# Kernel optimization log

Measured on AMD Instinct MI355X. Metric: run time of the kernel, lower is better.

Reference implementation:

```python
import jax, jax.numpy as jnp
import numpy as np

N = 100000
E = 1600000
IN_FEATS = 128
HIDDEN = 128
CLASSES = 64


def setup_inputs() -> dict:
    key = jax.random.key(0)
    ks = jax.random.split(key, 8)
    features = jax.random.normal(ks[0], (N, IN_FEATS), dtype=jnp.float32)
    edge_index = jax.random.randint(ks[1], (2, E), 0, N, dtype=jnp.int64 if jax.config.jax_enable_x64 else jnp.int32)
    # Glorot-init weights like PyG's GCNConv.lin, zero bias
    def glorot(k, fan_in, fan_out):
        lim = (6.0 / (fan_in + fan_out)) ** 0.5
        return jax.random.uniform(k, (fan_in, fan_out), dtype=jnp.float32, minval=-lim, maxval=lim)
    return {
        "features": features,
        "edge_index": edge_index,
        "W1": glorot(ks[2], IN_FEATS, HIDDEN), "b1": jnp.zeros((HIDDEN,), jnp.float32),
        "W2": glorot(ks[3], HIDDEN, HIDDEN), "b2": jnp.zeros((HIDDEN,), jnp.float32),
        "W3": glorot(ks[4], HIDDEN, CLASSES), "b3": jnp.zeros((CLASSES,), jnp.float32),
    }


def _gcn_conv(x, W, b, row, col, deg_norm_row, deg_norm_col):
    # x: [N, d_in] -> [N, d_out]. PyG GCNConv: linear first, then normalized aggregation, then bias.
    xw = x @ W                                   # [N, d_out]
    norm = deg_norm_row * deg_norm_col          # [E]
    msg = norm[:, None] * xw[row]               # gather from source nodes
    out = jax.ops.segment_sum(msg, col, num_segments=N)  # scatter-add to dst
    return out + b


def reference(features, edge_index, W1, b1, W2, b2, W3, b3):
    row, col = edge_index[0], edge_index[1]  # source -> target
    # gcn_norm with add_self_loops=False, unit edge weights: deg over dst nodes
    deg = jax.ops.segment_sum(jnp.ones((E,), features.dtype), col, num_segments=N)
    dinv = jnp.where(deg > 0, jax.lax.rsqrt(jnp.maximum(deg, 1.0)), 0.0)
    dn_row, dn_col = dinv[row], dinv[col]
    h = jax.nn.relu(_gcn_conv(features, W1, b1, row, col, dn_row, dn_col))
    h = jax.nn.relu(_gcn_conv(h, W2, b2, row, col, dn_row, dn_col))
    h = jax.nn.relu(_gcn_conv(h, W3, b3, row, col, dn_row, dn_col))
    return h
```

## Files before the change

### kernel.cpp

```cpp
#include <hip/hip_runtime.h>

#define ALIGNUP(x) (((x) + 255) & ~(size_t)255)
#define ABLK 256
#define BSHIFT 9

typedef _Float16 f16x8 __attribute__((ext_vector_type(8)));
typedef float f32x4 __attribute__((ext_vector_type(4)));


__global__ void bucket_hist_kernel(const int* __restrict__ col, unsigned* __restrict__ gHist,
                                   int nE, int chunk) {
    __shared__ unsigned hist[256];
    const int tid = threadIdx.x, blk = blockIdx.x;
    hist[tid] = 0;
    __syncthreads();
    const int e0 = blk * chunk, e1 = min(nE, e0 + chunk);
    for (int e = e0 + tid; e < e1; e += 256)
        atomicAdd(&hist[((unsigned)col[e]) >> BSHIFT], 1u);
    __syncthreads();
    gHist[tid * ABLK + blk] = hist[tid];
}

__global__ void bucket_scan_kernel(unsigned* __restrict__ g) {
    __shared__ unsigned ps[1024];
    const int tid = threadIdx.x;
    const int base = tid * 64;
    unsigned sum = 0;
    for (int k = 0; k < 64; ++k) sum += g[base + k];
    ps[tid] = sum;
    __syncthreads();
    for (int o = 1; o < 1024; o <<= 1) {
        unsigned t = tid >= o ? ps[tid - o] : 0u;
        __syncthreads();
        ps[tid] += t;
        __syncthreads();
    }
    unsigned run = ps[tid] - sum;
    for (int k = 0; k < 64; ++k) {
        unsigned v = g[base + k];
        g[base + k] = run;
        run += v;
    }
}

__global__ void bucket_scatter_kernel(const int* __restrict__ row, const int* __restrict__ col,
                                      const unsigned* __restrict__ gScan,
                                      unsigned* __restrict__ pairs, int nE, int chunk) {
    __shared__ unsigned basec[256];
    const int tid = threadIdx.x, blk = blockIdx.x;
    basec[tid] = gScan[tid * ABLK + blk];
    __syncthreads();
    const int e0 = blk * chunk, e1 = min(nE, e0 + chunk);
    for (int e = e0 + tid; e < e1; e += 256) {
        unsigned d = (unsigned)col[e];
        unsigned pos = atomicAdd(&basec[d >> BSHIFT], 1u);
        pairs[pos] = (((unsigned)row[e]) << BSHIFT) | (d & 511u);
    }
}

__global__ void bucket_sort_kernel(const unsigned* __restrict__ pairs,
                                   const unsigned* __restrict__ gScan,
                                   int* __restrict__ srcs, int* __restrict__ off,
                                   float* __restrict__ dinv, int nN, int nE) {
    __shared__ unsigned cnt[512], sc[512];
    const int tid = threadIdx.x, b = blockIdx.x;
    const unsigned s = gScan[b * ABLK];
    const unsigned t = (b + 1 < 256) ? gScan[(b + 1) * ABLK] : (unsigned)nE;
    cnt[tid] = 0;
    __syncthreads();
    for (unsigned i = s + tid; i < t; i += 512)
        atomicAdd(&cnt[pairs[i] & 511u], 1u);
    __syncthreads();
    const unsigned v = cnt[tid];
    sc[tid] = v;
    __syncthreads();
    for (int o = 1; o < 512; o <<= 1) {
        unsigned q = tid >= o ? sc[tid - o] : 0u;
        __syncthreads();
        sc[tid] += q;
        __syncthreads();
    }
    const unsigned excl = sc[tid] - v;
    const int node = b * 512 + tid;
    if (node < nN) {
        dinv[node] = v > 0 ? rsqrtf((float)v) : 0.f;
        off[node] = (int)(s + excl);
    }
    if (b == 0 && tid == 0) off[nN] = nE;
    sc[tid] = excl;
    __syncthreads();
    for (unsigned i = s + tid; i < t; i += 512) {
        unsigned p = pairs[i];
        unsigned pos = s + atomicAdd(&sc[p & 511u], 1u);
        srcs[pos] = (int)(p >> BSHIFT);
    }
}


template <int DOUT>
__global__ void wf_prep_kernel(const float* __restrict__ W, f16x8* __restrict__ Wf) {
    const int c = blockIdx.x * blockDim.x + threadIdx.x;
    if (c >= DOUT * 16) return;
    const int l = c & 63;
    const int fk = (c >> 6) & 3;
    const int j = c >> 8;
    const int n = j * 16 + (l & 15);
    const int kbase = fk * 32 + ((l >> 4) * 8);
    f16x8 v;
#pragma unroll
    for (int e = 0; e < 8; ++e)
        v[e] = (_Float16)W[(size_t)(kbase + e) * DOUT + n];
    Wf[c] = v;
}


template <int DOUT, bool AF32>
__launch_bounds__(256)
__global__ void gemm_mfma(const void* __restrict__ Xv, const f16x8* __restrict__ Wf,
                          const float* __restrict__ dinv, _Float16* __restrict__ Y, int nrows) {
    constexpr int NTILE = DOUT / 16;
    const int lane = threadIdx.x & 63;
    const int wvid = threadIdx.x >> 6;
    const int m = lane & 15;
    const int kb = lane >> 4;
    const int r0 = blockIdx.x * 64 + wvid * 16;
    if (r0 >= nrows) return;
    const int arow = min(r0 + m, nrows - 1);

    f16x8 a[4];
    if constexpr (AF32) {
        const float* Xp = (const float*)Xv + (size_t)arow * 128 + kb * 8;
#pragma unroll
        for (int k = 0; k < 4; ++k) {
            const float4 x0 = *(const float4*)(Xp + k * 32);
            const float4 x1 = *(const float4*)(Xp + k * 32 + 4);
            f16x8 t;
            t[0] = (_Float16)x0.x; t[1] = (_Float16)x0.y;
            t[2] = (_Float16)x0.z; t[3] = (_Float16)x0.w;
            t[4] = (_Float16)x1.x; t[5] = (_Float16)x1.y;
            t[6] = (_Float16)x1.z; t[7] = (_Float16)x1.w;
            a[k] = t;
        }
    } else {
        const _Float16* Xp = (const _Float16*)Xv + (size_t)arow * 128 + kb * 8;
#pragma unroll
        for (int k = 0; k < 4; ++k) a[k] = *(const f16x8*)(Xp + k * 32);
    }

    f32x4 acc[NTILE];
#pragma unroll
    for (int j = 0; j < NTILE; ++j) acc[j] = (f32x4){0.f, 0.f, 0.f, 0.f};
#pragma unroll
    for (int k = 0; k < 4; ++k)
#pragma unroll
        for (int j = 0; j < NTILE; ++j)
            acc[j] = __builtin_amdgcn_mfma_f32_16x16x32_f16(
                         a[k], Wf[(j * 4 + k) * 64 + lane], acc[j], 0, 0, 0);

#pragma unroll
    for (int i = 0; i < 4; ++i) {
        const int r = r0 + kb * 4 + i;
        if (r < nrows) {
            const float dv = dinv[r];
#pragma unroll
            for (int j = 0; j < NTILE; ++j)
                Y[(size_t)r * DOUT + j * 16 + m] = (_Float16)(acc[j][i] * dv);
        }
    }
}


template <int LD, typename OT>
__launch_bounds__(256)
__global__ void gather_grp(const _Float16* __restrict__ XW, const int* __restrict__ off,
                           const int* __restrict__ srcs, const float* __restrict__ dinv,
                           const float* __restrict__ bias, OT* __restrict__ out, int nN) {
    constexpr int G = 8, GPW = 8;
    const int half = blockIdx.y;
    XW   += half * 64;
    bias += half * 64;
    out  += half * 64;
    const int lane = threadIdx.x & 63;
    const int gl   = lane % G;
    const int grp  = lane / G;
    const int wid  = (blockIdx.x * blockDim.x + threadIdx.x) >> 6;
    const int nw   = (gridDim.x * blockDim.x) >> 6;

    for (int v0 = wid * GPW; v0 < nN; v0 += nw * GPW) {
        const int v   = v0 + grp;
        const bool act = v < nN;
        const int s0 = act ? off[v] : 0;
        const int s1 = act ? off[v + 1] : 0;
        float acc[8];
#pragma unroll
        for (int k = 0; k < 8; ++k) acc[k] = 0.f;

        int base = s0;
        while (base + G <= s1) {
            const int myidx = srcs[base + gl];
#pragma unroll
            for (int j = 0; j < G; ++j) {
                const int src = __shfl(myidx, grp * G + j);
                union { uint4 u; _Float16 h[8]; } cv;
                cv.u = *(const uint4*)(XW + (size_t)src * LD + gl * 8);
#pragma unroll
                for (int k = 0; k < 8; ++k) acc[k] += (float)cv.h[k];
            }
            base += G;
        }
        if (base < s1) {
            const int myidx = srcs[min(base + gl, s1 - 1)];
            const int rem = s1 - base;
            for (int j = 0; j < rem; ++j) {
                const int src = __shfl(myidx, grp * G + j);
                union { uint4 u; _Float16 h[8]; } cv;
                cv.u = *(const uint4*)(XW + (size_t)src * LD + gl * 8);
#pragma unroll
                for (int k = 0; k < 8; ++k) acc[k] += (float)cv.h[k];
            }
        }

        if (act) {
            const float dv = dinv[v];
            const float4 b0 = ((const float4*)bias)[gl * 2];
            const float4 b1 = ((const float4*)bias)[gl * 2 + 1];
            float o[8];
            o[0] = fmaxf(dv * acc[0] + b0.x, 0.f);
            o[1] = fmaxf(dv * acc[1] + b0.y, 0.f);
            o[2] = fmaxf(dv * acc[2] + b0.z, 0.f);
            o[3] = fmaxf(dv * acc[3] + b0.w, 0.f);
            o[4] = fmaxf(dv * acc[4] + b1.x, 0.f);
            o[5] = fmaxf(dv * acc[5] + b1.y, 0.f);
            o[6] = fmaxf(dv * acc[6] + b1.z, 0.f);
            o[7] = fmaxf(dv * acc[7] + b1.w, 0.f);
            if constexpr (sizeof(OT) == 2) {
                union { uint4 u; _Float16 h[8]; } ov;
#pragma unroll
                for (int k = 0; k < 8; ++k) ov.h[k] = (_Float16)o[k];
                *(uint4*)((_Float16*)out + (size_t)v * LD + gl * 8) = ov.u;
            } else {
                float* op = (float*)out + (size_t)v * LD + gl * 8;
                *(float4*)op       = make_float4(o[0], o[1], o[2], o[3]);
                *(float4*)(op + 4) = make_float4(o[4], o[5], o[6], o[7]);
            }
        }
    }
}

extern "C" void kernel_launch(void* const* d_in, const int* in_sizes, int n_in,
                              void* d_out, int out_size, void* d_ws, size_t ws_size,
                              hipStream_t stream) {
    const float* feats = (const float*)d_in[0];
    const int*   ei    = (const int*)d_in[1];
    const float* W1    = (const float*)d_in[2];
    const float* b1    = (const float*)d_in[3];
    const float* W2    = (const float*)d_in[4];
    const float* b2    = (const float*)d_in[5];
    const float* W3    = (const float*)d_in[6];
    const float* b3    = (const float*)d_in[7];

    const int N = in_sizes[0] / 128;
    const int E = in_sizes[1] / 2;
    const int* row = ei;
    const int* col = ei + E;

    char* p = (char*)d_ws;
    unsigned* gHist = (unsigned*)p; p += ALIGNUP((size_t)256 * ABLK * 4);
    float*     dinv = (float*)p;    p += ALIGNUP((size_t)N * 4);
    int*       off  = (int*)p;      p += ALIGNUP((size_t)(N + 1) * 4);
    int*       srcs = (int*)p;      p += ALIGNUP((size_t)E * 4);
    f16x8*     wf1  = (f16x8*)p;    p += ALIGNUP((size_t)128 * 16 * 16);
    f16x8*     wf2  = (f16x8*)p;    p += ALIGNUP((size_t)128 * 16 * 16);
    f16x8*     wf3  = (f16x8*)p;    p += ALIGNUP((size_t)64 * 16 * 16);
    _Float16*  bufW = (_Float16*)p; p += ALIGNUP((size_t)N * 128 * 2);
    _Float16*  bufX = (_Float16*)p;
    unsigned* pairs = (unsigned*)bufX;

    wf_prep_kernel<128><<<8, 256, 0, stream>>>(W1, wf1);
    wf_prep_kernel<128><<<8, 256, 0, stream>>>(W2, wf2);
    wf_prep_kernel<64><<<4, 256, 0, stream>>>(W3, wf3);

    const int chunk = (E + ABLK - 1) / ABLK;
    const int NB    = (N + 511) >> BSHIFT;
    bucket_hist_kernel<<<ABLK, 256, 0, stream>>>(col, gHist, E, chunk);
    bucket_scan_kernel<<<1, 1024, 0, stream>>>(gHist);
    bucket_scatter_kernel<<<ABLK, 256, 0, stream>>>(row, col, gHist, pairs, E, chunk);
    bucket_sort_kernel<<<NB, 512, 0, stream>>>(pairs, gHist, srcs, off, dinv, N, E);

    const int NCH = (N + 63) / 64;
    const int GBg = (N + 31) / 32;

    gemm_mfma<128, true><<<NCH, 256, 0, stream>>>(feats, wf1, dinv, bufW, N);
    gather_grp<128, _Float16><<<dim3(GBg, 2), 256, 0, stream>>>(bufW, off, srcs, dinv,
                                                                b1, bufX, N);
    gemm_mfma<128, false><<<NCH, 256, 0, stream>>>(bufX, wf2, dinv, bufW, N);
    gather_grp<128, _Float16><<<dim3(GBg, 2), 256, 0, stream>>>(bufW, off, srcs, dinv,
                                                                b2, bufX, N);
    gemm_mfma<64, false><<<NCH, 256, 0, stream>>>(bufX, wf3, dinv, bufW, N);
    gather_grp<64, float><<<dim3(GBg, 1), 256, 0, stream>>>(bufW, off, srcs, dinv, b3,
                                                            (float*)d_out, N);
}
```

Before: 282.9 us.

## Store GEMM output as 16-column planes and gather per-XCD slice

The GEMM now writes its output as separate planes of 16 fp16 columns, one plane per 16-column slice, instead of row-major. The gather kernel is rewritten so that consecutive block IDs cycle across slices (bid & (NSLICE-1)). Blocks of the same slice therefore land on the same XCD, and each XCD's L2 only has to hold one 3.2 MB plane rather than the whole feature matrix. In exchange each node's neighbour list is read once per slice, 32-byte gathers replace 128-byte rows, and per-wave parallelism per node shrinks to two lanes.

```diff
diff --git a/kernel.cpp b/kernel.cpp
--- a/kernel.cpp
+++ b/kernel.cpp
@@ -126,6 +126,7 @@
     const int r0 = blockIdx.x * 64 + wvid * 16;
     if (r0 >= nrows) return;
     const int arow = min(r0 + m, nrows - 1);
+    const size_t PS = (size_t)nrows * 16;
 
     f16x8 a[4];
     if constexpr (AF32) {
@@ -164,85 +165,77 @@
             const float dv = dinv[r];
 #pragma unroll
             for (int j = 0; j < NTILE; ++j)
-                Y[(size_t)r * DOUT + j * 16 + m] = (_Float16)(acc[j][i] * dv);
-        }
-    }
-}
-
-
-template <int LD, typename OT>
+                Y[(size_t)j * PS + (size_t)r * 16 + m] = (_Float16)(acc[j][i] * dv);
+        }
+    }
+}
+
+
+template <int NSLICE, typename OT>
 __launch_bounds__(256)
-__global__ void gather_grp(const _Float16* __restrict__ XW, const int* __restrict__ off,
+__global__ void gather_xcd(const _Float16* __restrict__ XWp, const int* __restrict__ off,
                            const int* __restrict__ srcs, const float* __restrict__ dinv,
                            const float* __restrict__ bias, OT* __restrict__ out, int nN) {
-    constexpr int G = 8, GPW = 8;
-    const int half = blockIdx.y;
-    XW   += half * 64;
-    bias += half * 64;
-    out  += half * 64;
-    const int lane = threadIdx.x & 63;
-    const int gl   = lane % G;
-    const int grp  = lane / G;
-    const int wid  = (blockIdx.x * blockDim.x + threadIdx.x) >> 6;
-    const int nw   = (gridDim.x * blockDim.x) >> 6;
-
-    for (int v0 = wid * GPW; v0 < nN; v0 += nw * GPW) {
-        const int v   = v0 + grp;
-        const bool act = v < nN;
-        const int s0 = act ? off[v] : 0;
-        const int s1 = act ? off[v + 1] : 0;
-        float acc[8];
-#pragma unroll
-        for (int k = 0; k < 8; ++k) acc[k] = 0.f;
-
-        int base = s0;
-        while (base + G <= s1) {
-            const int myidx = srcs[base + gl];
-#pragma unroll
-            for (int j = 0; j < G; ++j) {
-                const int src = __shfl(myidx, grp * G + j);
-                union { uint4 u; _Float16 h[8]; } cv;
-                cv.u = *(const uint4*)(XW + (size_t)src * LD + gl * 8);
-#pragma unroll
-                for (int k = 0; k < 8; ++k) acc[k] += (float)cv.h[k];
-            }
-            base += G;
-        }
-        if (base < s1) {
-            const int myidx = srcs[min(base + gl, s1 - 1)];
-            const int rem = s1 - base;
-            for (int j = 0; j < rem; ++j) {
-                const int src = __shfl(myidx, grp * G + j);
-                union { uint4 u; _Float16 h[8]; } cv;
-                cv.u = *(const uint4*)(XW + (size_t)src * LD + gl * 8);
-#pragma unroll
-                for (int k = 0; k < 8; ++k) acc[k] += (float)cv.h[k];
-            }
-        }
-
-        if (act) {
-            const float dv = dinv[v];
-            const float4 b0 = ((const float4*)bias)[gl * 2];
-            const float4 b1 = ((const float4*)bias)[gl * 2 + 1];
-            float o[8];
-            o[0] = fmaxf(dv * acc[0] + b0.x, 0.f);
-            o[1] = fmaxf(dv * acc[1] + b0.y, 0.f);
-            o[2] = fmaxf(dv * acc[2] + b0.z, 0.f);
-            o[3] = fmaxf(dv * acc[3] + b0.w, 0.f);
-            o[4] = fmaxf(dv * acc[4] + b1.x, 0.f);
-            o[5] = fmaxf(dv * acc[5] + b1.y, 0.f);
-            o[6] = fmaxf(dv * acc[6] + b1.z, 0.f);
-            o[7] = fmaxf(dv * acc[7] + b1.w, 0.f);
-            if constexpr (sizeof(OT) == 2) {
-                union { uint4 u; _Float16 h[8]; } ov;
-#pragma unroll
-                for (int k = 0; k < 8; ++k) ov.h[k] = (_Float16)o[k];
-                *(uint4*)((_Float16*)out + (size_t)v * LD + gl * 8) = ov.u;
-            } else {
-                float* op = (float*)out + (size_t)v * LD + gl * 8;
-                *(float4*)op       = make_float4(o[0], o[1], o[2], o[3]);
-                *(float4*)(op + 4) = make_float4(o[4], o[5], o[6], o[7]);
-            }
+    const int bid = blockIdx.x;
+    const int s = bid & (NSLICE - 1);
+    const int chunk = bid / NSLICE;
+    const int tid = threadIdx.x;
+    const int lane = tid & 63;
+    const int pl = lane & 1;
+    const int v = chunk * 128 + (tid >> 1);
+    const bool act = v < nN;
+
+    const _Float16* plane = XWp + (size_t)s * nN * 16;
+    const int s0 = act ? off[v] : 0;
+    const int s1 = act ? off[v + 1] : 0;
+
+    float acc[8];
+#pragma unroll
+    for (int k = 0; k < 8; ++k) acc[k] = 0.f;
+
+    int base = s0;
+    while (base + 2 <= s1) {
+        const int myidx = srcs[base + pl];
+#pragma unroll
+        for (int j = 0; j < 2; ++j) {
+            const int src = __shfl(myidx, (lane & 62) | j);
+            union { uint4 u; _Float16 h[8]; } cv;
+            cv.u = *(const uint4*)(plane + (size_t)src * 16 + pl * 8);
+#pragma unroll
+            for (int k = 0; k < 8; ++k) acc[k] += (float)cv.h[k];
+        }
+        base += 2;
+    }
+    if (base < s1) {
+        const int src = srcs[base];
+        union { uint4 u; _Float16 h[8]; } cv;
+        cv.u = *(const uint4*)(plane + (size_t)src * 16 + pl * 8);
+#pragma unroll
+        for (int k = 0; k < 8; ++k) acc[k] += (float)cv.h[k];
+    }
+
+    if (act) {
+        const float dv = dinv[v];
+        const float4 b0 = ((const float4*)bias)[s * 4 + pl * 2];
+        const float4 b1 = ((const float4*)bias)[s * 4 + pl * 2 + 1];
+        float o[8];
+        o[0] = fmaxf(dv * acc[0] + b0.x, 0.f);
+        o[1] = fmaxf(dv * acc[1] + b0.y, 0.f);
+        o[2] = fmaxf(dv * acc[2] + b0.z, 0.f);
+        o[3] = fmaxf(dv * acc[3] + b0.w, 0.f);
+        o[4] = fmaxf(dv * acc[4] + b1.x, 0.f);
+        o[5] = fmaxf(dv * acc[5] + b1.y, 0.f);
+        o[6] = fmaxf(dv * acc[6] + b1.z, 0.f);
+        o[7] = fmaxf(dv * acc[7] + b1.w, 0.f);
+        if constexpr (sizeof(OT) == 2) {
+            union { uint4 u; _Float16 h[8]; } ov;
+#pragma unroll
+            for (int k = 0; k < 8; ++k) ov.h[k] = (_Float16)o[k];
+            *(uint4*)((_Float16*)out + (size_t)v * (NSLICE * 16) + s * 16 + pl * 8) = ov.u;
+        } else {
+            float* op = (float*)out + (size_t)v * (NSLICE * 16) + s * 16 + pl * 8;
+            *(float4*)op       = make_float4(o[0], o[1], o[2], o[3]);
+            *(float4*)(op + 4) = make_float4(o[4], o[5], o[6], o[7]);
         }
     }
 }
@@ -287,16 +280,14 @@
     bucket_scatter_kernel<<<ABLK, 256, 0, stream>>>(row, col, gHist, pairs, E, chunk);
     bucket_sort_kernel<<<NB, 512, 0, stream>>>(pairs, gHist, srcs, off, dinv, N, E);
 
-    const int NCH = (N + 63) / 64;
-    const int GBg = (N + 31) / 32;
+    const int NCH  = (N + 63) / 64;
+    const int NCG  = (N + 127) / 128;
 
     gemm_mfma<128, true><<<NCH, 256, 0, stream>>>(feats, wf1, dinv, bufW, N);
-    gather_grp<128, _Float16><<<dim3(GBg, 2), 256, 0, stream>>>(bufW, off, srcs, dinv,
-                                                                b1, bufX, N);
+    gather_xcd<8, _Float16><<<NCG * 8, 256, 0, stream>>>(bufW, off, srcs, dinv, b1, bufX, N);
     gemm_mfma<128, false><<<NCH, 256, 0, stream>>>(bufX, wf2, dinv, bufW, N);
-    gather_grp<128, _Float16><<<dim3(GBg, 2), 256, 0, stream>>>(bufW, off, srcs, dinv,
-                                                                b2, bufX, N);
+    gather_xcd<8, _Float16><<<NCG * 8, 256, 0, stream>>>(bufW, off, srcs, dinv, b2, bufX, N);
     gemm_mfma<64, false><<<NCH, 256, 0, stream>>>(bufX, wf3, dinv, bufW, N);
-    gather_grp<64, float><<<dim3(GBg, 1), 256, 0, stream>>>(bufW, off, srcs, dinv, b3,
-                                                            (float*)d_out, N);
-}
+    gather_xcd<4, float><<<NCG * 4, 256, 0, stream>>>(bufW, off, srcs, dinv, b3,
+                                                      (float*)d_out, N);
+}
```

Result: slower. 404.4 us (+43.0%).
